# Optimization experiments

Hardware: AMD Instinct MI355X
Metric: run time of the kernel (lower is better)

Reference implementation:

```python
import jax, jax.numpy as jnp
import numpy as np

N = 8192
LAYER_WIDTHS = [32, 64, 32]
LAYER_CENTERS = [512, 512]


def setup_inputs() -> dict:
    key = jax.random.key(0)
    ks = jax.random.split(key, 8)
    inp = {"x": jax.random.normal(ks[0], (N, LAYER_WIDTHS[0]), dtype=jnp.float32)}
    # layer 0 params
    inp["centers0"] = jax.random.normal(ks[1], (LAYER_CENTERS[0], LAYER_WIDTHS[0]), dtype=jnp.float32)
    inp["log_sigmas0"] = jnp.zeros((LAYER_CENTERS[0],), dtype=jnp.float32)
    lim0 = 1.0 / np.sqrt(LAYER_CENTERS[0])
    inp["W0"] = jax.random.uniform(ks[2], (LAYER_WIDTHS[1], LAYER_CENTERS[0]), jnp.float32, -lim0, lim0)
    inp["b0"] = jax.random.uniform(ks[3], (LAYER_WIDTHS[1],), jnp.float32, -lim0, lim0)
    # layer 1 params
    inp["centers1"] = jax.random.normal(ks[4], (LAYER_CENTERS[1], LAYER_WIDTHS[1]), dtype=jnp.float32)
    inp["log_sigmas1"] = jnp.zeros((LAYER_CENTERS[1],), dtype=jnp.float32)
    lim1 = 1.0 / np.sqrt(LAYER_CENTERS[1])
    inp["W1"] = jax.random.uniform(ks[5], (LAYER_WIDTHS[2], LAYER_CENTERS[1]), jnp.float32, -lim1, lim1)
    inp["b1"] = jax.random.uniform(ks[6], (LAYER_WIDTHS[2],), jnp.float32, -lim1, lim1)
    return inp


def _rbf(h, centers, log_sigmas):
    # h: [N, in], centers: [C, in] -> [N, C]
    diff = h[:, None, :] - centers[None, :, :]            # [N, C, in]
    dist = jnp.sqrt(jnp.sum(diff * diff, axis=-1))        # [N, C]
    d = dist / jnp.exp(log_sigmas)[None, :]
    return jnp.exp(-(d * d))                              # gaussian basis


def reference(x, centers0, log_sigmas0, W0, b0, centers1, log_sigmas1, W1, b1):
    h = _rbf(x, centers0, log_sigmas0) @ W0.T + b0        # [N, widths[1]]
    h = _rbf(h, centers1, log_sigmas1) @ W1.T + b1        # [N, widths[2]]
    return h
```

## Files before the change

### kernel.cpp

```cpp
#include <hip/hip_runtime.h>
#include <math.h>


#define NROWS 8192
#define R 16
#define BLOCK 512
#define GRID (NROWS / R)

typedef __attribute__((ext_vector_type(8))) short short8;
typedef __attribute__((ext_vector_type(4))) float f32x4;

__device__ __forceinline__ short bf16t(float f) {
    return (short)(__float_as_uint(f) >> 16);
}

__global__ __launch_bounds__(BLOCK, 4)
void rbfnet(const float* __restrict__ x,
            const float* __restrict__ c0, const float* __restrict__ ls0,
            const float* __restrict__ W0, const float* __restrict__ b0,
            const float* __restrict__ c1, const float* __restrict__ ls1,
            const float* __restrict__ W1, const float* __restrict__ b1,
            float* __restrict__ out)
{
    __shared__ unsigned short phi_u[16 * 520];
    __shared__ float h_lds[16][68];
    __shared__ float htmp[2][16][68];
    __shared__ float otmp[4][16][36];
    __shared__ float rn_lds[16], hn_lds[16];

    const int t  = threadIdx.x;
    const int l  = t & 63;
    const int w  = t >> 6;
    const int mr = l & 15;
    const int kg = l >> 4;
    const int row0 = blockIdx.x * R;

    short8 ax;
    {
        const float4 x0 = *(const float4*)&x[(row0 + mr) * 32 + kg * 8];
        const float4 x1 = *(const float4*)&x[(row0 + mr) * 32 + kg * 8 + 4];
        const float xo[8] = {x0.x, x0.y, x0.z, x0.w, x1.x, x1.y, x1.z, x1.w};
        float rp = 0.f;
        #pragma unroll
        for (int i = 0; i < 8; ++i) { ax[i] = bf16t(xo[i]); rp += xo[i] * xo[i]; }
        rp += __shfl_xor(rp, 16);
        rp += __shfl_xor(rp, 32);
        if (t < 16) rn_lds[t] = rp;
    }
    __syncthreads();

    {
        float rnv[4];
        #pragma unroll
        for (int g = 0; g < 4; ++g) rnv[g] = rn_lds[kg * 4 + g];
        #pragma unroll 1
        for (int q = 0; q < 4; ++q) {
            const int c = 64 * w + 16 * q + mr;
            const float4 cv0 = *(const float4*)&c0[c * 32 + kg * 8];
            const float4 cv1 = *(const float4*)&c0[c * 32 + kg * 8 + 4];
            const float co[8] = {cv0.x, cv0.y, cv0.z, cv0.w, cv1.x, cv1.y, cv1.z, cv1.w};
            short8 bc;
            float cp = 0.f;
            #pragma unroll
            for (int i = 0; i < 8; ++i) { bc[i] = bf16t(co[i]); cp += co[i] * co[i]; }
            cp += __shfl_xor(cp, 16);
            cp += __shfl_xor(cp, 32);
            f32x4 d = {0.f, 0.f, 0.f, 0.f};
            d = __builtin_amdgcn_mfma_f32_16x16x32_bf16(ax, bc, d, 0, 0, 0);
            const float iv = __expf(-2.0f * ls0[c]);
            #pragma unroll
            for (int g = 0; g < 4; ++g) {
                const float p = __expf(-(rnv[g] + cp - 2.f * d[g]) * iv);
                phi_u[(kg * 4 + g) * 520 + c] = (unsigned short)bf16t(p);
            }
        }
    }
    __syncthreads();

    {
        const int half = w >> 2;
        const int j = 16 * (w & 3) + mr;
        f32x4 hD = {0.f, 0.f, 0.f, 0.f};
        #pragma unroll 1
        for (int ks = 8 * half; ks < 8 * half + 8; ++ks) {
            const short8 ap = *(const short8*)&phi_u[mr * 520 + 32 * ks + kg * 8];
            const float4 w0v = *(const float4*)&W0[j * 512 + 32 * ks + kg * 8];
            const float4 w1v = *(const float4*)&W0[j * 512 + 32 * ks + kg * 8 + 4];
            const float wo[8] = {w0v.x, w0v.y, w0v.z, w0v.w, w1v.x, w1v.y, w1v.z, w1v.w};
            short8 bw;
            #pragma unroll
            for (int i = 0; i < 8; ++i) bw[i] = bf16t(wo[i]);
            hD = __builtin_amdgcn_mfma_f32_16x16x32_bf16(ap, bw, hD, 0, 0, 0);
        }
        #pragma unroll
        for (int g = 0; g < 4; ++g) htmp[half][kg * 4 + g][j] = hD[g];
    }
    __syncthreads();

    {
        const int j = t & 63;
        const int r0 = t >> 6;
        const float bj = b0[j];
        #pragma unroll
        for (int rr = 0; rr < 2; ++rr) {
            const int r = r0 + 8 * rr;
            h_lds[r][j] = htmp[0][r][j] + htmp[1][r][j] + bj;
        }
    }
    __syncthreads();
    {
        const int r = t >> 5, d = t & 31;
        const float v0 = h_lds[r][d], v1 = h_lds[r][d + 32];
        float s = v0 * v0 + v1 * v1;
        s += __shfl_xor(s, 1);  s += __shfl_xor(s, 2);  s += __shfl_xor(s, 4);
        s += __shfl_xor(s, 8);  s += __shfl_xor(s, 16);
        if (d == 0) hn_lds[r] = s;
    }
    __syncthreads();

    {
        short8 ah0, ah1;
        {
            const float4 h0 = *(const float4*)&h_lds[mr][kg * 8];
            const float4 h1 = *(const float4*)&h_lds[mr][kg * 8 + 4];
            const float4 h2 = *(const float4*)&h_lds[mr][32 + kg * 8];
            const float4 h3 = *(const float4*)&h_lds[mr][32 + kg * 8 + 4];
            ah0[0]=bf16t(h0.x); ah0[1]=bf16t(h0.y); ah0[2]=bf16t(h0.z); ah0[3]=bf16t(h0.w);
            ah0[4]=bf16t(h1.x); ah0[5]=bf16t(h1.y); ah0[6]=bf16t(h1.z); ah0[7]=bf16t(h1.w);
            ah1[0]=bf16t(h2.x); ah1[1]=bf16t(h2.y); ah1[2]=bf16t(h2.z); ah1[3]=bf16t(h2.w);
            ah1[4]=bf16t(h3.x); ah1[5]=bf16t(h3.y); ah1[6]=bf16t(h3.z); ah1[7]=bf16t(h3.w);
        }
        float hnv[4];
        #pragma unroll
        for (int g = 0; g < 4; ++g) hnv[g] = hn_lds[kg * 4 + g];
        #pragma unroll 1
        for (int q = 0; q < 4; ++q) {
            const int c = 64 * w + 16 * q + mr;
            const float4 a0 = *(const float4*)&c1[c * 64 + kg * 8];
            const float4 a1 = *(const float4*)&c1[c * 64 + kg * 8 + 4];
            const float4 a2 = *(const float4*)&c1[c * 64 + 32 + kg * 8];
            const float4 a3 = *(const float4*)&c1[c * 64 + 32 + kg * 8 + 4];
            const float co[16] = {a0.x,a0.y,a0.z,a0.w, a1.x,a1.y,a1.z,a1.w,
                                  a2.x,a2.y,a2.z,a2.w, a3.x,a3.y,a3.z,a3.w};
            short8 bc0, bc1;
            float cp = 0.f;
            #pragma unroll
            for (int i = 0; i < 8; ++i)  { bc0[i] = bf16t(co[i]);     cp += co[i] * co[i]; }
            #pragma unroll
            for (int i = 0; i < 8; ++i)  { bc1[i] = bf16t(co[8 + i]); cp += co[8+i] * co[8+i]; }
            cp += __shfl_xor(cp, 16);
            cp += __shfl_xor(cp, 32);
            f32x4 d = {0.f, 0.f, 0.f, 0.f};
            d = __builtin_amdgcn_mfma_f32_16x16x32_bf16(ah0, bc0, d, 0, 0, 0);
            d = __builtin_amdgcn_mfma_f32_16x16x32_bf16(ah1, bc1, d, 0, 0, 0);
            const float iv = __expf(-2.0f * ls1[c]);
            #pragma unroll
            for (int g = 0; g < 4; ++g) {
                const float p = __expf(-(hnv[g] + cp - 2.f * d[g]) * iv);
                phi_u[(kg * 4 + g) * 520 + c] = (unsigned short)bf16t(p);
            }
        }
    }
    __syncthreads();

    {
        const int qtr = w >> 1;
        const int j = 16 * (w & 1) + mr;
        f32x4 oD = {0.f, 0.f, 0.f, 0.f};
        #pragma unroll 1
        for (int ks = 4 * qtr; ks < 4 * qtr + 4; ++ks) {
            const short8 ap = *(const short8*)&phi_u[mr * 520 + 32 * ks + kg * 8];
            const float4 w0v = *(const float4*)&W1[j * 512 + 32 * ks + kg * 8];
            const float4 w1v = *(const float4*)&W1[j * 512 + 32 * ks + kg * 8 + 4];
            const float wo[8] = {w0v.x, w0v.y, w0v.z, w0v.w, w1v.x, w1v.y, w1v.z, w1v.w};
            short8 bw;
            #pragma unroll
            for (int i = 0; i < 8; ++i) bw[i] = bf16t(wo[i]);
            oD = __builtin_amdgcn_mfma_f32_16x16x32_bf16(ap, bw, oD, 0, 0, 0);
        }
        #pragma unroll
        for (int g = 0; g < 4; ++g) otmp[qtr][kg * 4 + g][j] = oD[g];
    }
    __syncthreads();

    {
        const int r = t >> 5, j = t & 31;
        const float s = otmp[0][r][j] + otmp[1][r][j] + otmp[2][r][j] + otmp[3][r][j] + b1[j];
        out[(row0 + r) * 32 + j] = s;
    }
}

extern "C" void kernel_launch(void* const* d_in, const int* in_sizes, int n_in,
                              void* d_out, int out_size, void* d_ws, size_t ws_size,
                              hipStream_t stream) {
    const float* xin = (const float*)d_in[0];
    const float* c0  = (const float*)d_in[1];
    const float* ls0 = (const float*)d_in[2];
    const float* W0  = (const float*)d_in[3];
    const float* b0  = (const float*)d_in[4];
    const float* c1  = (const float*)d_in[5];
    const float* ls1 = (const float*)d_in[6];
    const float* W1  = (const float*)d_in[7];
    const float* b1  = (const float*)d_in[8];
    float* outp = (float*)d_out;

    hipLaunchKernelGGL(rbfnet, dim3(GRID), dim3(BLOCK), 0, stream,
                       xin, c0, ls0, W0, b0, c1, ls1, W1, b1, outp);
}
```

Baseline: 92.37 us.

## Prepack weights and centers into bf16 MFMA fragment layout in a pre-kernel

Adds a prepack kernel that converts centers and weight matrices to bf16 in the exact per-lane MFMA fragment order, and precomputes center squared norms and inverse sigma factors. The main kernel then loads ready-made short8 fragments instead of reloading fp32 data, converting it and computing norms in all 512 blocks. It also removes two barriers by sharing row norms through shuffles and fusing the bias add, norm and bf16 conversion of h into one pass. The cost is a second kernel launch plus a workspace round trip on every call.

```diff
diff --git a/kernel.cpp b/kernel.cpp
--- a/kernel.cpp
+++ b/kernel.cpp
@@ -3,9 +3,8 @@
 
 
 #define NROWS 8192
-#define R 16
 #define BLOCK 512
-#define GRID (NROWS / R)
+#define GRID (NROWS / 16)
 
 typedef __attribute__((ext_vector_type(8))) short short8;
 typedef __attribute__((ext_vector_type(4))) float f32x4;
@@ -14,28 +13,70 @@
     return (short)(__float_as_uint(f) >> 16);
 }
 
+__global__ void prepack(const float* __restrict__ c0, const float* __restrict__ ls0,
+                        const float* __restrict__ W0,
+                        const float* __restrict__ c1, const float* __restrict__ ls1,
+                        const float* __restrict__ W1,
+                        unsigned short* __restrict__ wpc0, unsigned short* __restrict__ wpc1,
+                        unsigned short* __restrict__ wpw0, unsigned short* __restrict__ wpw1,
+                        float2* __restrict__ cniv0, float2* __restrict__ cniv1)
+{
+    const int i = blockIdx.x * 256 + threadIdx.x;
+    if (i < 16384) {
+        const int e = i & 7, l = (i >> 3) & 63, nt = i >> 9;
+        const int c = nt * 16 + (l & 15), k = (l >> 4) * 8 + e;
+        wpc0[i] = (unsigned short)bf16t(c0[c * 32 + k]);
+    } else if (i < 49152) {
+        const int j = i - 16384;
+        const int e = j & 7, l = (j >> 3) & 63, kk = (j >> 9) & 1, nt = j >> 10;
+        const int c = nt * 16 + (l & 15), k = kk * 32 + (l >> 4) * 8 + e;
+        wpc1[j] = (unsigned short)bf16t(c1[c * 64 + k]);
+    } else if (i < 81920) {
+        const int j = i - 49152;
+        const int e = j & 7, l = (j >> 3) & 63, nt = (j >> 9) & 3, ks = j >> 11;
+        const int col = nt * 16 + (l & 15), k = ks * 32 + (l >> 4) * 8 + e;
+        wpw0[j] = (unsigned short)bf16t(W0[col * 512 + k]);
+    } else if (i < 98304) {
+        const int j = i - 81920;
+        const int e = j & 7, l = (j >> 3) & 63, nt = (j >> 9) & 1, ks = j >> 10;
+        const int col = nt * 16 + (l & 15), k = ks * 32 + (l >> 4) * 8 + e;
+        wpw1[j] = (unsigned short)bf16t(W1[col * 512 + k]);
+    } else if (i < 98304 + 512) {
+        const int c = i - 98304;
+        float s = 0.f;
+        for (int d = 0; d < 32; ++d) { const float v = c0[c * 32 + d]; s += v * v; }
+        cniv0[c] = make_float2(s, __expf(-2.0f * ls0[c]));
+    } else if (i < 98304 + 1024) {
+        const int c = i - 98816;
+        float s = 0.f;
+        for (int d = 0; d < 64; ++d) { const float v = c1[c * 64 + d]; s += v * v; }
+        cniv1[c] = make_float2(s, __expf(-2.0f * ls1[c]));
+    }
+}
+
 __global__ __launch_bounds__(BLOCK, 4)
 void rbfnet(const float* __restrict__ x,
-            const float* __restrict__ c0, const float* __restrict__ ls0,
-            const float* __restrict__ W0, const float* __restrict__ b0,
-            const float* __restrict__ c1, const float* __restrict__ ls1,
-            const float* __restrict__ W1, const float* __restrict__ b1,
+            const float* __restrict__ b0, const float* __restrict__ b1,
+            const unsigned short* __restrict__ wpc0, const unsigned short* __restrict__ wpc1,
+            const unsigned short* __restrict__ wpw0, const unsigned short* __restrict__ wpw1,
+            const float2* __restrict__ cniv0, const float2* __restrict__ cniv1,
             float* __restrict__ out)
 {
     __shared__ unsigned short phi_u[16 * 520];
-    __shared__ float h_lds[16][68];
+    __shared__ unsigned short hfrag[16 * 72];
     __shared__ float htmp[2][16][68];
     __shared__ float otmp[4][16][36];
-    __shared__ float rn_lds[16], hn_lds[16];
+    __shared__ float hn_lds[16];
 
     const int t  = threadIdx.x;
     const int l  = t & 63;
     const int w  = t >> 6;
     const int mr = l & 15;
     const int kg = l >> 4;
-    const int row0 = blockIdx.x * R;
+    const int row0 = blockIdx.x * 16;
 
     short8 ax;
+    float rnv[4];
     {
         const float4 x0 = *(const float4*)&x[(row0 + mr) * 32 + kg * 8];
         const float4 x1 = *(const float4*)&x[(row0 + mr) * 32 + kg * 8 + 4];
@@ -45,141 +86,91 @@
         for (int i = 0; i < 8; ++i) { ax[i] = bf16t(xo[i]); rp += xo[i] * xo[i]; }
         rp += __shfl_xor(rp, 16);
         rp += __shfl_xor(rp, 32);
-        if (t < 16) rn_lds[t] = rp;
-    }
-    __syncthreads();
-
-    {
-        float rnv[4];
-        #pragma unroll
-        for (int g = 0; g < 4; ++g) rnv[g] = rn_lds[kg * 4 + g];
-        #pragma unroll 1
+        #pragma unroll
+        for (int g = 0; g < 4; ++g) rnv[g] = __shfl(rp, 4 * kg + g);
+    }
+
+    {
+        #pragma unroll 2
         for (int q = 0; q < 4; ++q) {
-            const int c = 64 * w + 16 * q + mr;
-            const float4 cv0 = *(const float4*)&c0[c * 32 + kg * 8];
-            const float4 cv1 = *(const float4*)&c0[c * 32 + kg * 8 + 4];
-            const float co[8] = {cv0.x, cv0.y, cv0.z, cv0.w, cv1.x, cv1.y, cv1.z, cv1.w};
-            short8 bc;
-            float cp = 0.f;
-            #pragma unroll
-            for (int i = 0; i < 8; ++i) { bc[i] = bf16t(co[i]); cp += co[i] * co[i]; }
-            cp += __shfl_xor(cp, 16);
-            cp += __shfl_xor(cp, 32);
+            const int nt = 4 * w + q;
+            const int c  = nt * 16 + mr;
+            const short8 bc = *(const short8*)&wpc0[(nt * 64 + l) * 8];
+            const float2 cv = cniv0[c];
             f32x4 d = {0.f, 0.f, 0.f, 0.f};
             d = __builtin_amdgcn_mfma_f32_16x16x32_bf16(ax, bc, d, 0, 0, 0);
-            const float iv = __expf(-2.0f * ls0[c]);
             #pragma unroll
             for (int g = 0; g < 4; ++g) {
-                const float p = __expf(-(rnv[g] + cp - 2.f * d[g]) * iv);
-                phi_u[(kg * 4 + g) * 520 + c] = (unsigned short)bf16t(p);
+                const float p = __expf(-(rnv[g] + cv.x - 2.f * d[g]) * cv.y);
+                phi_u[(4 * kg + g) * 520 + c] = (unsigned short)bf16t(p);
             }
         }
     }
     __syncthreads();
 
     {
-        const int half = w >> 2;
-        const int j = 16 * (w & 3) + mr;
+        const int nt = w & 3, half = w >> 2;
         f32x4 hD = {0.f, 0.f, 0.f, 0.f};
-        #pragma unroll 1
+        #pragma unroll 2
         for (int ks = 8 * half; ks < 8 * half + 8; ++ks) {
-            const short8 ap = *(const short8*)&phi_u[mr * 520 + 32 * ks + kg * 8];
-            const float4 w0v = *(const float4*)&W0[j * 512 + 32 * ks + kg * 8];
-            const float4 w1v = *(const float4*)&W0[j * 512 + 32 * ks + kg * 8 + 4];
-            const float wo[8] = {w0v.x, w0v.y, w0v.z, w0v.w, w1v.x, w1v.y, w1v.z, w1v.w};
-            short8 bw;
-            #pragma unroll
-            for (int i = 0; i < 8; ++i) bw[i] = bf16t(wo[i]);
+            const short8 ap = *(const short8*)&phi_u[mr * 520 + ks * 32 + kg * 8];
+            const short8 bw = *(const short8*)&wpw0[((ks * 4 + nt) * 64 + l) * 8];
             hD = __builtin_amdgcn_mfma_f32_16x16x32_bf16(ap, bw, hD, 0, 0, 0);
         }
         #pragma unroll
-        for (int g = 0; g < 4; ++g) htmp[half][kg * 4 + g][j] = hD[g];
-    }
-    __syncthreads();
-
-    {
-        const int j = t & 63;
-        const int r0 = t >> 6;
-        const float bj = b0[j];
-        #pragma unroll
-        for (int rr = 0; rr < 2; ++rr) {
-            const int r = r0 + 8 * rr;
-            h_lds[r][j] = htmp[0][r][j] + htmp[1][r][j] + bj;
-        }
-    }
-    __syncthreads();
-    {
-        const int r = t >> 5, d = t & 31;
-        const float v0 = h_lds[r][d], v1 = h_lds[r][d + 32];
-        float s = v0 * v0 + v1 * v1;
+        for (int g = 0; g < 4; ++g) htmp[half][4 * kg + g][nt * 16 + mr] = hD[g];
+    }
+    __syncthreads();
+
+    {
+        const int r = t >> 5, dd = t & 31;
+        const float h0 = htmp[0][r][dd]      + htmp[1][r][dd]      + b0[dd];
+        const float h1 = htmp[0][r][dd + 32] + htmp[1][r][dd + 32] + b0[dd + 32];
+        hfrag[r * 72 + dd]      = (unsigned short)bf16t(h0);
+        hfrag[r * 72 + 32 + dd] = (unsigned short)bf16t(h1);
+        float s = h0 * h0 + h1 * h1;
         s += __shfl_xor(s, 1);  s += __shfl_xor(s, 2);  s += __shfl_xor(s, 4);
         s += __shfl_xor(s, 8);  s += __shfl_xor(s, 16);
-        if (d == 0) hn_lds[r] = s;
-    }
-    __syncthreads();
-
-    {
-        short8 ah0, ah1;
-        {
-            const float4 h0 = *(const float4*)&h_lds[mr][kg * 8];
-            const float4 h1 = *(const float4*)&h_lds[mr][kg * 8 + 4];
-            const float4 h2 = *(const float4*)&h_lds[mr][32 + kg * 8];
-            const float4 h3 = *(const float4*)&h_lds[mr][32 + kg * 8 + 4];
-            ah0[0]=bf16t(h0.x); ah0[1]=bf16t(h0.y); ah0[2]=bf16t(h0.z); ah0[3]=bf16t(h0.w);
-            ah0[4]=bf16t(h1.x); ah0[5]=bf16t(h1.y); ah0[6]=bf16t(h1.z); ah0[7]=bf16t(h1.w);
-            ah1[0]=bf16t(h2.x); ah1[1]=bf16t(h2.y); ah1[2]=bf16t(h2.z); ah1[3]=bf16t(h2.w);
-            ah1[4]=bf16t(h3.x); ah1[5]=bf16t(h3.y); ah1[6]=bf16t(h3.z); ah1[7]=bf16t(h3.w);
-        }
+        if (dd == 0) hn_lds[r] = s;
+    }
+    __syncthreads();
+
+    {
+        const short8 ah0 = *(const short8*)&hfrag[mr * 72 + kg * 8];
+        const short8 ah1 = *(const short8*)&hfrag[mr * 72 + 32 + kg * 8];
         float hnv[4];
         #pragma unroll
-        for (int g = 0; g < 4; ++g) hnv[g] = hn_lds[kg * 4 + g];
-        #pragma unroll 1
+        for (int g = 0; g < 4; ++g) hnv[g] = hn_lds[4 * kg + g];
+        #pragma unroll 2
         for (int q = 0; q < 4; ++q) {
-            const int c = 64 * w + 16 * q + mr;
-            const float4 a0 = *(const float4*)&c1[c * 64 + kg * 8];
-            const float4 a1 = *(const float4*)&c1[c * 64 + kg * 8 + 4];
-            const float4 a2 = *(const float4*)&c1[c * 64 + 32 + kg * 8];
-            const float4 a3 = *(const float4*)&c1[c * 64 + 32 + kg * 8 + 4];
-            const float co[16] = {a0.x,a0.y,a0.z,a0.w, a1.x,a1.y,a1.z,a1.w,
-                                  a2.x,a2.y,a2.z,a2.w, a3.x,a3.y,a3.z,a3.w};
-            short8 bc0, bc1;
-            float cp = 0.f;
-            #pragma unroll
-            for (int i = 0; i < 8; ++i)  { bc0[i] = bf16t(co[i]);     cp += co[i] * co[i]; }
-            #pragma unroll
-            for (int i = 0; i < 8; ++i)  { bc1[i] = bf16t(co[8 + i]); cp += co[8+i] * co[8+i]; }
-            cp += __shfl_xor(cp, 16);
-            cp += __shfl_xor(cp, 32);
+            const int nt = 4 * w + q;
+            const int c  = nt * 16 + mr;
+            const short8 bc0 = *(const short8*)&wpc1[((nt * 2 + 0) * 64 + l) * 8];
+            const short8 bc1 = *(const short8*)&wpc1[((nt * 2 + 1) * 64 + l) * 8];
+            const float2 cv = cniv1[c];
             f32x4 d = {0.f, 0.f, 0.f, 0.f};
             d = __builtin_amdgcn_mfma_f32_16x16x32_bf16(ah0, bc0, d, 0, 0, 0);
             d = __builtin_amdgcn_mfma_f32_16x16x32_bf16(ah1, bc1, d, 0, 0, 0);
-            const float iv = __expf(-2.0f * ls1[c]);
             #pragma unroll
             for (int g = 0; g < 4; ++g) {
-                const float p = __expf(-(hnv[g] + cp - 2.f * d[g]) * iv);
-                phi_u[(kg * 4 + g) * 520 + c] = (unsigned short)bf16t(p);
+                const float p = __expf(-(hnv[g] + cv.x - 2.f * d[g]) * cv.y);
+                phi_u[(4 * kg + g) * 520 + c] = (unsigned short)bf16t(p);
             }
         }
     }
     __syncthreads();
 
     {
-        const int qtr = w >> 1;
-        const int j = 16 * (w & 1) + mr;
+        const int nt = w & 1, qtr = w >> 1;
         f32x4 oD = {0.f, 0.f, 0.f, 0.f};
-        #pragma unroll 1
+        #pragma unroll 2
         for (int ks = 4 * qtr; ks < 4 * qtr + 4; ++ks) {
-            const short8 ap = *(const short8*)&phi_u[mr * 520 + 32 * ks + kg * 8];
-            const float4 w0v = *(const float4*)&W1[j * 512 + 32 * ks + kg * 8];
-            const float4 w1v = *(const float4*)&W1[j * 512 + 32 * ks + kg * 8 + 4];
-            const float wo[8] = {w0v.x, w0v.y, w0v.z, w0v.w, w1v.x, w1v.y, w1v.z, w1v.w};
-            short8 bw;
-            #pragma unroll
-            for (int i = 0; i < 8; ++i) bw[i] = bf16t(wo[i]);
+            const short8 ap = *(const short8*)&phi_u[mr * 520 + ks * 32 + kg * 8];
+            const short8 bw = *(const short8*)&wpw1[((ks * 2 + nt) * 64 + l) * 8];
             oD = __builtin_amdgcn_mfma_f32_16x16x32_bf16(ap, bw, oD, 0, 0, 0);
         }
         #pragma unroll
-        for (int g = 0; g < 4; ++g) otmp[qtr][kg * 4 + g][j] = oD[g];
+        for (int g = 0; g < 4; ++g) otmp[qtr][4 * kg + g][nt * 16 + mr] = oD[g];
     }
     __syncthreads();
 
@@ -204,6 +195,16 @@
     const float* b1  = (const float*)d_in[8];
     float* outp = (float*)d_out;
 
+    char* ws = (char*)d_ws;
+    unsigned short* wpc0 = (unsigned short*)(ws);
+    unsigned short* wpc1 = (unsigned short*)(ws + 32768);
+    unsigned short* wpw0 = (unsigned short*)(ws + 98304);
+    unsigned short* wpw1 = (unsigned short*)(ws + 163840);
+    float2* cniv0 = (float2*)(ws + 196608);
+    float2* cniv1 = (float2*)(ws + 200704);
+
+    hipLaunchKernelGGL(prepack, dim3(388), dim3(256), 0, stream,
+                       c0, ls0, W0, c1, ls1, W1, wpc0, wpc1, wpw0, wpw1, cniv0, cniv1);
     hipLaunchKernelGGL(rbfnet, dim3(GRID), dim3(BLOCK), 0, stream,
-                       xin, c0, ls0, W0, b0, c1, ls1, W1, b1, outp);
-}
+                       xin, b0, b1, wpc0, wpc1, wpw0, wpw1, cniv0, cniv1, outp);
+}
```

Result: faster. 79.08 us (-14.4%).
